# Optimization experiments

Hardware: AMD Instinct MI355X
Metric: run time of the kernel (lower is better)

Reference implementation:

```python
import jax, jax.numpy as jnp
import numpy as np

# ---- static ragged feature layout (from CTGAN metadata) ----
NUM_CLUSTERS = [10, 8, 10, 5, 10, 10, 7, 10, 10, 10]          # per numerical feature
NUM_CATEGORIES = [2, 5, 10, 3, 50, 4, 2, 8, 100, 6, 2, 3, 12, 5, 2, 30, 4, 9, 2, 7]
TAU = 0.2        # GumbelSoftmax temperature (teras default)
BN_EPS = 1e-3    # keras BatchNormalization default epsilon
LATENT_DIM = 128
BATCH = 65536

_seg, _alpha = [], []
_gid = 0
for c in NUM_CLUSTERS:
    _seg.append(_gid); _alpha.append(True); _gid += 1        # alpha scalar (tanh), own segment
    _seg += [_gid] * c; _alpha += [False] * c; _gid += 1     # beta cluster group (gumbel softmax)
for k in NUM_CATEGORIES:
    _seg += [_gid] * k; _alpha += [False] * k; _gid += 1     # categorical group (gumbel softmax)
SEG = jnp.asarray(np.array(_seg, dtype=np.int32))
ALPHA_MASK = jnp.asarray(np.array(_alpha, dtype=bool))
N_SEG = _gid
DATA_DIM = len(_seg)  # 366


def setup_inputs() -> dict:
    key = jax.random.key(0)
    ks = jax.random.split(key, 8)
    z = jax.random.normal(ks[0], (BATCH, LATENT_DIM), dtype=jnp.float32)
    # pre-sampled standard Gumbel noise for the gumbel-softmax groups
    u = jax.random.uniform(ks[1], (BATCH, DATA_DIM), dtype=jnp.float32, minval=1e-6, maxval=1.0 - 1e-6)
    g = -jnp.log(-jnp.log(u))
    def w(k, fi, fo):
        return jax.random.normal(k, (fi, fo), dtype=jnp.float32) * (1.0 / np.sqrt(fi))
    return {
        "z": z, "g": g,
        "W1": w(ks[2], LATENT_DIM, 256), "b1": jnp.zeros((256,), jnp.float32),
        "gamma1": jnp.ones((256,), jnp.float32), "beta1": jnp.zeros((256,), jnp.float32),
        "W2": w(ks[3], LATENT_DIM + 256, 256), "b2": jnp.zeros((256,), jnp.float32),
        "gamma2": jnp.ones((256,), jnp.float32), "beta2": jnp.zeros((256,), jnp.float32),
        "Wout": w(ks[4], LATENT_DIM + 512, DATA_DIM), "bout": jnp.zeros((DATA_DIM,), jnp.float32),
    }


def _bn_relu(h, gamma, beta):
    # training-mode batch norm (batch statistics), as used while training CTGAN
    mu = jnp.mean(h, axis=0)
    var = jnp.var(h, axis=0)
    return jax.nn.relu((h - mu) * jax.lax.rsqrt(var + BN_EPS) * gamma + beta)


def reference(z, g, W1, b1, gamma1, beta1, W2, b2, gamma2, beta2, Wout, bout):
    # CTGAN residual generator layers: out = concat([relu(bn(dense(x))), x])
    h1 = jnp.concatenate([_bn_relu(z @ W1 + b1, gamma1, beta1), z], axis=1)    # [B, 384]
    h2 = jnp.concatenate([_bn_relu(h1 @ W2 + b2, gamma2, beta2), h1], axis=1)  # [B, 640]
    logits = h2 @ Wout + bout                                                  # [B, 366]

    # ragged per-group gumbel-softmax: segment-wise stable softmax over columns
    zt = ((logits + g) / TAU).T                                   # [D, B]
    m = jax.ops.segment_max(zt, SEG, num_segments=N_SEG)          # [S, B]
    e = jnp.exp(zt - m[SEG])
    s = jax.ops.segment_sum(e, SEG, num_segments=N_SEG)
    soft = (e / s[SEG]).T                                         # [B, D]
    # alpha columns: tanh of raw logits; all other columns: group softmax
    return jnp.where(ALPHA_MASK[None, :], jnp.tanh(logits), soft)
```

## Files before the change

kernel.cpp:

```cpp
#include <hip/hip_runtime.h>

typedef _Float16 half_t;
typedef _Float16 half4 __attribute__((ext_vector_type(4)));
typedef _Float16 half8 __attribute__((ext_vector_type(8)));
typedef float f32x4 __attribute__((ext_vector_type(4)));

#define AS1 __attribute__((address_space(1)))
#define AS3 __attribute__((address_space(3)))

static constexpr int NBATCH = 65536;

__device__ __forceinline__ bool is_alpha(int c) {
  const unsigned long long AM0 =
      (1ull << 0) | (1ull << 11) | (1ull << 20) | (1ull << 31) | (1ull << 37) |
      (1ull << 48) | (1ull << 59);
  const unsigned long long AM1 = (1ull << 3) | (1ull << 14) | (1ull << 25);
  if (c >= 90) return false;
  return (((c < 64) ? (AM0 >> c) : (AM1 >> (c - 64))) & 1ull) != 0ull;
}

__global__ __launch_bounds__(256) void k_cvtz(const float* __restrict__ z,
                                              half_t* __restrict__ dst) {
  size_t i = (size_t)blockIdx.x * 256 + threadIdx.x;
  int row = (int)(i >> 4), c8 = (int)(i & 15) << 3;
  const float* s = z + (size_t)row * 128 + c8;
  float4 v0 = *(const float4*)s;
  float4 v1 = *(const float4*)(s + 4);
  half8 h;
  h[0]=(half_t)v0.x; h[1]=(half_t)v0.y; h[2]=(half_t)v0.z; h[3]=(half_t)v0.w;
  h[4]=(half_t)v1.x; h[5]=(half_t)v1.y; h[6]=(half_t)v1.z; h[7]=(half_t)v1.w;
  *(half8*)(dst + (size_t)row * 640 + c8) = h;
}

__global__ __launch_bounds__(256) void k_transpose(const float* __restrict__ W,
                                                   half_t* __restrict__ Wt,
                                                   int K, int N, int total) {
  int i = blockIdx.x * 256 + threadIdx.x;
  if (i >= total) return;
  int n = i / K;
  int k = i - n * K;
  float v = (n < N) ? W[k * N + n] : 0.f;
  Wt[i] = (half_t)v;
}

template<bool STATS, bool F16OUT>
__global__ __launch_bounds__(256) void k_gemm(
    const half_t* __restrict__ A, int lda, int K,
    const half_t* __restrict__ Bt,
    const float* __restrict__ bias,
    half_t* __restrict__ o16, float* __restrict__ o32, int ldo, int ncreal,
    float* __restrict__ ps, float* __restrict__ pq) {
  __shared__ __align__(16) char smem[32768];
  const int tid  = threadIdx.x;
  const int lane = tid & 63;
  const int w    = tid >> 6;
  const int wr   = w >> 1, wc = w & 1;
  const int ml   = lane & 15, g = lane >> 4;
  const int brow = blockIdx.x * 128;
  const int bcol = blockIdx.y * 128;
  const int sr  = lane >> 3;
  const int scg = (lane & 7) ^ sr;

  f32x4 acc[4][4];
#pragma unroll
  for (int i = 0; i < 4; i++)
#pragma unroll
    for (int j = 0; j < 4; j++) acc[i][j] = (f32x4){0.f, 0.f, 0.f, 0.f};

  const half_t* Abase = A  + (size_t)brow * lda;
  const half_t* Bbase = Bt + (size_t)bcol * K;
  const int nt = K >> 6;

  half_t* As = (half_t*)smem;
  half_t* Bs = (half_t*)(smem + 16384);

  for (int t = 0; t < nt; t++) {
    const int k0 = t * 64;
    if (t) __syncthreads();
#pragma unroll
    for (int it = 0; it < 4; it++) {
      int q = it * 4 + w;
      int r = q * 8 + sr;
      __builtin_amdgcn_global_load_lds(
          (AS1 const void*)(Abase + (size_t)r * lda + k0 + scg * 8),
          (AS3 void*)(As + q * 512), 16, 0, 0);
      __builtin_amdgcn_global_load_lds(
          (AS1 const void*)(Bbase + (size_t)r * K + k0 + scg * 8),
          (AS3 void*)(Bs + q * 512), 16, 0, 0);
    }
    __syncthreads();
#pragma unroll
    for (int t2 = 0; t2 < 2; t2++) {
      const int c4 = t2 * 4 + g;
      half8 af[4], bf[4];
#pragma unroll
      for (int fm = 0; fm < 4; fm++) {
        int row = wr * 64 + fm * 16 + ml;
        af[fm] = *(const half8*)((const char*)As + row * 128 + ((c4 ^ (row & 7)) << 4));
      }
#pragma unroll
      for (int fn = 0; fn < 4; fn++) {
        int row = wc * 64 + fn * 16 + ml;
        bf[fn] = *(const half8*)((const char*)Bs + row * 128 + ((c4 ^ (row & 7)) << 4));
      }
#pragma unroll
      for (int fm = 0; fm < 4; fm++)
#pragma unroll
        for (int fn = 0; fn < 4; fn++)
          acc[fm][fn] = __builtin_amdgcn_mfma_f32_16x16x32_f16(af[fm], bf[fn], acc[fm][fn], 0, 0, 0);
    }
  }
  __syncthreads();

#pragma unroll
  for (int fn = 0; fn < 4; fn++) {
    int col  = wc * 64 + fn * 16 + ml;
    int gcol = bcol + col;
    float bz = (gcol < ncreal) ? bias[gcol] : 0.f;
    float s = 0.f, q = 0.f;
#pragma unroll
    for (int fm = 0; fm < 4; fm++)
#pragma unroll
      for (int rr = 0; rr < 4; rr++) {
        float v = acc[fm][fn][rr] + bz;
        acc[fm][fn][rr] = v;
        if (STATS) { s += v; q += v * v; }
      }
    if (STATS) {
      s += __shfl_xor(s, 16, 64); s += __shfl_xor(s, 32, 64);
      q += __shfl_xor(q, 16, 64); q += __shfl_xor(q, 32, 64);
      if (g == 0) {
        ps[(size_t)gcol * 1024 + blockIdx.x * 2 + wr] = s;
        pq[(size_t)gcol * 1024 + blockIdx.x * 2 + wr] = q;
      }
    }
  }

  if (F16OUT) {
    half_t* so = (half_t*)smem;
#pragma unroll
    for (int fn = 0; fn < 4; fn++)
#pragma unroll
      for (int fm = 0; fm < 4; fm++)
#pragma unroll
        for (int rr = 0; rr < 4; rr++)
          so[(wr * 64 + fm * 16 + g * 4 + rr) * 128 + wc * 64 + fn * 16 + ml] =
              (half_t)acc[fm][fn][rr];
    __syncthreads();
#pragma unroll
    for (int it = 0; it < 8; it++) {
      int r = it * 16 + (tid >> 4);
      int c = (tid & 15) * 8;
      *(half8*)(o16 + (size_t)(brow + r) * ldo + bcol + c) = *(const half8*)&so[r * 128 + c];
    }
  } else {
    float* so = (float*)smem;
    for (int h = 0; h < 2; h++) {
      if (wr == h) {
#pragma unroll
        for (int fn = 0; fn < 4; fn++)
#pragma unroll
          for (int fm = 0; fm < 4; fm++)
#pragma unroll
            for (int rr = 0; rr < 4; rr++)
              so[(fm * 16 + g * 4 + rr) * 128 + wc * 64 + fn * 16 + ml] = acc[fm][fn][rr];
      }
      __syncthreads();
      int r0 = h * 64;
      for (int i = tid; i < 64 * 64; i += 256) {
        int r  = i >> 6;
        int c2 = (i & 63) * 2;
        int gc = bcol + c2;
        if (gc < ncreal) {
          float2 v = *(const float2*)&so[r * 128 + c2];
          if (gc < 90) {
            if (is_alpha(gc))     v.x = tanhf(v.x);
            if (is_alpha(gc + 1)) v.y = tanhf(v.y);
          }
          *(float2*)(o32 + (size_t)(brow + r0 + r) * ldo + gc) = v;
        }
      }
      __syncthreads();
    }
  }
}

__global__ __launch_bounds__(256) void k_bnfinal(
    const float* __restrict__ ps, const float* __restrict__ pq,
    const float* __restrict__ gamma, const float* __restrict__ beta,
    float* __restrict__ sc, float* __restrict__ sh) {
  int c = blockIdx.x, t = threadIdx.x;
  float s = 0.f, q = 0.f;
#pragma unroll
  for (int i = 0; i < 4; i++) {
    s += ps[(size_t)c * 1024 + t + i * 256];
    q += pq[(size_t)c * 1024 + t + i * 256];
  }
#pragma unroll
  for (int o = 1; o < 64; o <<= 1) { s += __shfl_xor(s, o, 64); q += __shfl_xor(q, o, 64); }
  __shared__ float ss[4], qq[4];
  if ((t & 63) == 0) { ss[t >> 6] = s; qq[t >> 6] = q; }
  __syncthreads();
  if (t == 0) {
    s = ss[0] + ss[1] + ss[2] + ss[3];
    q = qq[0] + qq[1] + qq[2] + qq[3];
    float mu   = s * (1.f / NBATCH);
    float var  = fmaxf(q * (1.f / NBATCH) - mu * mu, 0.f);
    float rstd = rsqrtf(var + 1e-3f);
    float a = gamma[c] * rstd;
    sc[c] = a;
    sh[c] = beta[c] - mu * a;
  }
}

__global__ __launch_bounds__(256) void k_bnrelu(half_t* __restrict__ p,
                                                const float* __restrict__ sc,
                                                const float* __restrict__ sh) {
  size_t i = (size_t)blockIdx.x * 256 + threadIdx.x;
  int row = (int)(i >> 5), c8 = (int)(i & 31) << 3;
  half_t* a = p + (size_t)row * 640 + c8;
  half8 v = *(const half8*)a;
  half8 o;
#pragma unroll
  for (int j = 0; j < 8; j++)
    o[j] = (half_t)fmaxf(fmaf((float)v[j], sc[c8 + j], sh[c8 + j]), 0.f);
  *(half8*)a = o;
}

template<int L>
__device__ __forceinline__ void seg_norm(float* __restrict__ zr, int S, int Lr) {
  float v[L];
#pragma unroll
  for (int j = 0; j < L; j++) v[j] = (j < Lr) ? zr[S + j] : -1e30f;
  float m = -1e30f;
#pragma unroll
  for (int j = 0; j < L; j++) m = fmaxf(m, v[j]);
  float s = 0.f;
#pragma unroll
  for (int j = 0; j < L; j++) { float e = __expf(v[j] - m); v[j] = e; s += e; }
  const float inv = 1.0f / s;
#pragma unroll
  for (int j = 0; j < L; j++)
    if (j < Lr) zr[S + j] = v[j] * inv;
}

template<int H>
__device__ __forceinline__ void seg_quad(float* __restrict__ zr, int base, int n) {
  float v[H];
#pragma unroll
  for (int j = 0; j < H; j++) v[j] = (j < n) ? zr[base + j] : -1e30f;
  float m = -1e30f;
#pragma unroll
  for (int j = 0; j < H; j++) m = fmaxf(m, v[j]);
  m = fmaxf(m, __shfl_xor(m, 1, 64));
  m = fmaxf(m, __shfl_xor(m, 2, 64));
  float s = 0.f;
#pragma unroll
  for (int j = 0; j < H; j++) { float e = __expf(v[j] - m); v[j] = e; s += e; }
  s += __shfl_xor(s, 1, 64);
  s += __shfl_xor(s, 2, 64);
  const float inv = 1.0f / s;
#pragma unroll
  for (int j = 0; j < H; j++)
    if (j < n) zr[base + j] = v[j] * inv;
}

__global__ __launch_bounds__(256, 6) void k_softmax(const float* __restrict__ g,
                                                    float* __restrict__ out) {
  __shared__ float zb[16][373];
  const int tid = threadIdx.x;
  const size_t gbase = (size_t)blockIdx.x * 16 * 366;
  for (int i2 = tid; i2 < 16 * 183; i2 += 256) {
    int e0 = i2 * 2;
    int r = e0 / 366;
    int c = e0 - r * 366;
    float2 lg = *(const float2*)(out + gbase + e0);
    float2 gg = *(const float2*)(g + gbase + e0);
    zb[r][c]     = is_alpha(c)     ? lg.x : (lg.x + gg.x) * 5.0f;
    zb[r][c + 1] = is_alpha(c + 1) ? lg.y : (lg.y + gg.y) * 5.0f;
  }
  __syncthreads();
  {
    const int lane = tid & 63;
    const int w    = tid >> 6;
    const int quad = lane & 3;
    float* zr = &zb[lane >> 2][0];
    switch (w) {
      case 0:
        seg_quad<25>(zr, 184 + quad * 25, 25);
        break;
      case 1:
        seg_quad<13>(zr, 120 + quad * 13 - (quad >> 1) * (quad & 1), 13 - (quad >> 1));
        seg_quad<8>(zr, 314 + quad * 8 - (quad >> 1) * (quad & 1), 8 - (quad >> 1));
        break;
      case 2: {
        int s0 = (quad == 0) ? 295 : (quad == 1) ? 107 : (quad == 2) ? 38 : 68;
        int l0 = (quad == 0) ? 12 : 10;
        int s1 = (quad == 0) ? 1 : (quad == 1) ? 21 : (quad == 2) ? 49 : 79;
        int s2 = (quad == 0) ? 0 : (quad == 1) ? 100 : (quad == 2) ? 174 : 290;
        int l2 = (quad == 0) ? 0 : 2;
        seg_norm<12>(zr, s0, l0);
        seg_norm<10>(zr, s1, 10);
        seg_norm<2>(zr, s2, l2);
        break;
      }
      default: {
        int s0 = (quad == 0) ? 90 : (quad == 1) ? 12 : (quad == 2) ? 60 : 102;
        int l0 = (quad == 0) ? 10 : (quad == 1) ? 8 : (quad == 2) ? 7 : 5;
        int s1 = (quad == 0) ? 348 : (quad == 1) ? 176 : (quad == 2) ? 359 : 307;
        int l1 = (quad == 0) ? 9 : (quad == 1) ? 8 : (quad == 2) ? 7 : 5;
        int s2 = (quad == 0) ? 312 : (quad == 1) ? 284 : (quad == 2) ? 32 : 170;
        int l2 = (quad == 0) ? 2 : (quad == 1) ? 6 : (quad == 2) ? 5 : 4;
        int s3 = (quad == 0) ? 117 : (quad == 1) ? 357 : (quad == 2) ? 292 : 344;
        int l3 = (quad == 0) ? 3 : (quad == 1) ? 2 : (quad == 2) ? 3 : 4;
        seg_norm<10>(zr, s0, l0);
        seg_norm<9>(zr, s1, l1);
        seg_norm<6>(zr, s2, l2);
        seg_norm<4>(zr, s3, l3);
        break;
      }
    }
  }
  __syncthreads();
  for (int i2 = tid; i2 < 16 * 183; i2 += 256) {
    int e0 = i2 * 2;
    int r = e0 / 366;
    int c = e0 - r * 366;
    float2 v;
    v.x = zb[r][c];
    v.y = zb[r][c + 1];
    *(float2*)(out + gbase + e0) = v;
  }
}

extern "C" void kernel_launch(void* const* d_in, const int* in_sizes, int n_in,
                              void* d_out, int out_size, void* d_ws, size_t ws_size,
                              hipStream_t stream) {
  const float* z      = (const float*)d_in[0];
  const float* g      = (const float*)d_in[1];
  const float* W1     = (const float*)d_in[2];
  const float* b1     = (const float*)d_in[3];
  const float* gamma1 = (const float*)d_in[4];
  const float* beta1  = (const float*)d_in[5];
  const float* W2     = (const float*)d_in[6];
  const float* b2     = (const float*)d_in[7];
  const float* gamma2 = (const float*)d_in[8];
  const float* beta2  = (const float*)d_in[9];
  const float* Wout   = (const float*)d_in[10];
  const float* bout   = (const float*)d_in[11];
  float* out = (float*)d_out;
  char* ws = (char*)d_ws;

  size_t off = 0;
  half_t* act = (half_t*)(ws + off); off += (size_t)NBATCH * 640 * 2;
  half_t* W1t = (half_t*)(ws + off); off += (size_t)256 * 128 * 2;
  half_t* W2t = (half_t*)(ws + off); off += (size_t)256 * 384 * 2;
  half_t* Wot = (half_t*)(ws + off); off += (size_t)384 * 640 * 2;
  float*  ps  = (float*)(ws + off);  off += (size_t)256 * 1024 * 4;
  float*  pq  = (float*)(ws + off);  off += (size_t)256 * 1024 * 4;
  float*  sc1 = (float*)(ws + off);  off += 256 * 4;
  float*  sh1 = (float*)(ws + off);  off += 256 * 4;
  float*  sc2 = (float*)(ws + off);  off += 256 * 4;
  float*  sh2 = (float*)(ws + off);  off += 256 * 4;
  (void)ws_size; (void)in_sizes; (void)n_in; (void)out_size;

  k_cvtz<<<4096, 256, 0, stream>>>(z, act + 512);
  k_transpose<<<(256 * 128 + 255) / 256, 256, 0, stream>>>(W1, W1t, 128, 256, 256 * 128);
  k_transpose<<<(256 * 384 + 255) / 256, 256, 0, stream>>>(W2, W2t, 384, 256, 256 * 384);
  k_transpose<<<(384 * 640 + 255) / 256, 256, 0, stream>>>(Wout, Wot, 640, 366, 384 * 640);

  k_gemm<true, true><<<dim3(512, 2), 256, 0, stream>>>(
      act + 512, 640, 128, W1t, b1, act + 256, nullptr, 640, 256, ps, pq);
  k_bnfinal<<<256, 256, 0, stream>>>(ps, pq, gamma1, beta1, sc1, sh1);
  k_bnrelu<<<8192, 256, 0, stream>>>(act + 256, sc1, sh1);

  k_gemm<true, true><<<dim3(512, 2), 256, 0, stream>>>(
      act + 256, 640, 384, W2t, b2, act + 0, nullptr, 640, 256, ps, pq);
  k_bnfinal<<<256, 256, 0, stream>>>(ps, pq, gamma2, beta2, sc2, sh2);
  k_bnrelu<<<8192, 256, 0, stream>>>(act + 0, sc2, sh2);

  k_gemm<false, false><<<dim3(512, 3), 256, 0, stream>>>(
      act, 640, 640, Wot, bout, nullptr, out, 366, 366, nullptr, nullptr);

  k_softmax<<<NBATCH / 16, 256, 0, stream>>>(g, out);
}
```

Before: 201.4 us.

## Fuse BN+ReLU into next GEMM's A-fragment load and emit fp16 logits

Removes the two standalone BN+ReLU passes over the activation buffer. The per-column affine and ReLU are applied to A fragments inside the following GEMM, using fp16 scale, shift and clamp tables; identity tables cover the raw-z and h1 pass-through columns. The output GEMM now writes fp16 logits (with tanh on alpha columns) into a padded scratch buffer that the softmax kernel reads, instead of writing fp32 into the output. This cuts global traffic and kernel launches, at the cost of extra VALU work per tile, fp16 rounding of the BN parameters and logits, and the same BN being recomputed for every tile.

```diff
diff --git a/kernel.cpp b/kernel.cpp
--- a/kernel.cpp
+++ b/kernel.cpp
@@ -17,6 +17,13 @@
   const unsigned long long AM1 = (1ull << 3) | (1ull << 14) | (1ull << 25);
   if (c >= 90) return false;
   return (((c < 64) ? (AM0 >> c) : (AM1 >> (c - 64))) & 1ull) != 0ull;
+}
+
+__device__ __forceinline__ half8 bn8(half8 x, half8 sc, half8 sh, half8 lo) {
+  half8 r = x * sc + sh;
+#pragma unroll
+  for (int j = 0; j < 8; j++) r[j] = (r[j] < lo[j]) ? lo[j] : r[j];
+  return r;
 }
 
 __global__ __launch_bounds__(256) void k_cvtz(const float* __restrict__ z,
@@ -43,12 +50,19 @@
   Wt[i] = (half_t)v;
 }
 
-template<bool STATS, bool F16OUT>
+__global__ void k_identtab(half_t* sc, half_t* sh, half_t* lo, int n) {
+  int t = blockIdx.x * 128 + threadIdx.x;
+  if (t < n) { sc[t] = (half_t)1.f; sh[t] = (half_t)0.f; lo[t] = (half_t)(-65504.f); }
+}
+
+template<bool STATS, bool TRANS, bool ALPHA>
 __global__ __launch_bounds__(256) void k_gemm(
     const half_t* __restrict__ A, int lda, int K,
     const half_t* __restrict__ Bt,
     const float* __restrict__ bias,
-    half_t* __restrict__ o16, float* __restrict__ o32, int ldo, int ncreal,
+    const half_t* __restrict__ tsc, const half_t* __restrict__ tsh,
+    const half_t* __restrict__ tlo,
+    half_t* __restrict__ o16, int ldo, int ncreal,
     float* __restrict__ ps, float* __restrict__ pq) {
   __shared__ __align__(16) char smem[32768];
   const int tid  = threadIdx.x;
@@ -76,6 +90,12 @@
 
   for (int t = 0; t < nt; t++) {
     const int k0 = t * 64;
+    half8 sc0, sh0, lo0, sc1, sh1, lo1;
+    if (TRANS) {
+      const int ka = k0 + g * 8, kb = k0 + 32 + g * 8;
+      sc0 = *(const half8*)&tsc[ka]; sh0 = *(const half8*)&tsh[ka]; lo0 = *(const half8*)&tlo[ka];
+      sc1 = *(const half8*)&tsc[kb]; sh1 = *(const half8*)&tsh[kb]; lo1 = *(const half8*)&tlo[kb];
+    }
     if (t) __syncthreads();
 #pragma unroll
     for (int it = 0; it < 4; it++) {
@@ -98,6 +118,13 @@
         int row = wr * 64 + fm * 16 + ml;
         af[fm] = *(const half8*)((const char*)As + row * 128 + ((c4 ^ (row & 7)) << 4));
       }
+      if (TRANS) {
+        const half8 sc = t2 ? sc1 : sc0;
+        const half8 sh = t2 ? sh1 : sh0;
+        const half8 lo = t2 ? lo1 : lo0;
+#pragma unroll
+        for (int fm = 0; fm < 4; fm++) af[fm] = bn8(af[fm], sc, sh, lo);
+      }
 #pragma unroll
       for (int fn = 0; fn < 4; fn++) {
         int row = wc * 64 + fn * 16 + ml;
@@ -118,13 +145,15 @@
     int gcol = bcol + col;
     float bz = (gcol < ncreal) ? bias[gcol] : 0.f;
     float s = 0.f, q = 0.f;
+    const bool al = ALPHA && (gcol < 90) && is_alpha(gcol);
 #pragma unroll
     for (int fm = 0; fm < 4; fm++)
 #pragma unroll
       for (int rr = 0; rr < 4; rr++) {
         float v = acc[fm][fn][rr] + bz;
+        if (STATS) { s += v; q += v * v; }
+        if (al) v = tanhf(v);
         acc[fm][fn][rr] = v;
-        if (STATS) { s += v; q += v * v; }
       }
     if (STATS) {
       s += __shfl_xor(s, 16, 64); s += __shfl_xor(s, 32, 64);
@@ -136,59 +165,29 @@
     }
   }
 
-  if (F16OUT) {
-    half_t* so = (half_t*)smem;
-#pragma unroll
-    for (int fn = 0; fn < 4; fn++)
-#pragma unroll
-      for (int fm = 0; fm < 4; fm++)
-#pragma unroll
-        for (int rr = 0; rr < 4; rr++)
-          so[(wr * 64 + fm * 16 + g * 4 + rr) * 128 + wc * 64 + fn * 16 + ml] =
-              (half_t)acc[fm][fn][rr];
-    __syncthreads();
-#pragma unroll
-    for (int it = 0; it < 8; it++) {
-      int r = it * 16 + (tid >> 4);
-      int c = (tid & 15) * 8;
-      *(half8*)(o16 + (size_t)(brow + r) * ldo + bcol + c) = *(const half8*)&so[r * 128 + c];
-    }
-  } else {
-    float* so = (float*)smem;
-    for (int h = 0; h < 2; h++) {
-      if (wr == h) {
-#pragma unroll
-        for (int fn = 0; fn < 4; fn++)
-#pragma unroll
-          for (int fm = 0; fm < 4; fm++)
-#pragma unroll
-            for (int rr = 0; rr < 4; rr++)
-              so[(fm * 16 + g * 4 + rr) * 128 + wc * 64 + fn * 16 + ml] = acc[fm][fn][rr];
-      }
-      __syncthreads();
-      int r0 = h * 64;
-      for (int i = tid; i < 64 * 64; i += 256) {
-        int r  = i >> 6;
-        int c2 = (i & 63) * 2;
-        int gc = bcol + c2;
-        if (gc < ncreal) {
-          float2 v = *(const float2*)&so[r * 128 + c2];
-          if (gc < 90) {
-            if (is_alpha(gc))     v.x = tanhf(v.x);
-            if (is_alpha(gc + 1)) v.y = tanhf(v.y);
-          }
-          *(float2*)(o32 + (size_t)(brow + r0 + r) * ldo + gc) = v;
-        }
-      }
-      __syncthreads();
-    }
+  half_t* so = (half_t*)smem;
+#pragma unroll
+  for (int fn = 0; fn < 4; fn++)
+#pragma unroll
+    for (int fm = 0; fm < 4; fm++)
+#pragma unroll
+      for (int rr = 0; rr < 4; rr++)
+        so[(wr * 64 + fm * 16 + g * 4 + rr) * 128 + wc * 64 + fn * 16 + ml] =
+            (half_t)acc[fm][fn][rr];
+  __syncthreads();
+#pragma unroll
+  for (int it = 0; it < 8; it++) {
+    int r = it * 16 + (tid >> 4);
+    int c = (tid & 15) * 8;
+    *(half8*)(o16 + (size_t)(brow + r) * ldo + bcol + c) = *(const half8*)&so[r * 128 + c];
   }
 }
 
 __global__ __launch_bounds__(256) void k_bnfinal(
     const float* __restrict__ ps, const float* __restrict__ pq,
     const float* __restrict__ gamma, const float* __restrict__ beta,
-    float* __restrict__ sc, float* __restrict__ sh) {
+    half_t* __restrict__ scA, half_t* __restrict__ shA, half_t* __restrict__ loA,
+    half_t* __restrict__ scB, half_t* __restrict__ shB, half_t* __restrict__ loB) {
   int c = blockIdx.x, t = threadIdx.x;
   float s = 0.f, q = 0.f;
 #pragma unroll
@@ -207,24 +206,11 @@
     float mu   = s * (1.f / NBATCH);
     float var  = fmaxf(q * (1.f / NBATCH) - mu * mu, 0.f);
     float rstd = rsqrtf(var + 1e-3f);
-    float a = gamma[c] * rstd;
-    sc[c] = a;
-    sh[c] = beta[c] - mu * a;
-  }
-}
-
-__global__ __launch_bounds__(256) void k_bnrelu(half_t* __restrict__ p,
-                                                const float* __restrict__ sc,
-                                                const float* __restrict__ sh) {
-  size_t i = (size_t)blockIdx.x * 256 + threadIdx.x;
-  int row = (int)(i >> 5), c8 = (int)(i & 31) << 3;
-  half_t* a = p + (size_t)row * 640 + c8;
-  half8 v = *(const half8*)a;
-  half8 o;
-#pragma unroll
-  for (int j = 0; j < 8; j++)
-    o[j] = (half_t)fmaxf(fmaf((float)v[j], sc[c8 + j], sh[c8 + j]), 0.f);
-  *(half8*)a = o;
+    float a  = gamma[c] * rstd;
+    float sh = beta[c] - mu * a;
+    scA[c] = (half_t)a; shA[c] = (half_t)sh; loA[c] = (half_t)0.f;
+    if (scB) { scB[c] = (half_t)a; shB[c] = (half_t)sh; loB[c] = (half_t)0.f; }
+  }
 }
 
 template<int L>
@@ -265,19 +251,22 @@
     if (j < n) zr[base + j] = v[j] * inv;
 }
 
-__global__ __launch_bounds__(256, 6) void k_softmax(const float* __restrict__ g,
+__global__ __launch_bounds__(256, 6) void k_softmax(const half_t* __restrict__ lg,
+                                                    const float* __restrict__ g,
                                                     float* __restrict__ out) {
   __shared__ float zb[16][373];
-  const int tid = threadIdx.x;
-  const size_t gbase = (size_t)blockIdx.x * 16 * 366;
+  const int tid  = threadIdx.x;
+  const int row0 = blockIdx.x * 16;
+  const size_t gbase = (size_t)row0 * 366;
   for (int i2 = tid; i2 < 16 * 183; i2 += 256) {
     int e0 = i2 * 2;
     int r = e0 / 366;
     int c = e0 - r * 366;
-    float2 lg = *(const float2*)(out + gbase + e0);
+    const half_t* lp = lg + (size_t)(row0 + r) * 384 + c;
+    float lx = (float)lp[0], ly = (float)lp[1];
     float2 gg = *(const float2*)(g + gbase + e0);
-    zb[r][c]     = is_alpha(c)     ? lg.x : (lg.x + gg.x) * 5.0f;
-    zb[r][c + 1] = is_alpha(c + 1) ? lg.y : (lg.y + gg.y) * 5.0f;
+    zb[r][c]     = is_alpha(c)     ? lx : (lx + gg.x) * 5.0f;
+    zb[r][c + 1] = is_alpha(c + 1) ? ly : (ly + gg.y) * 5.0f;
   }
   __syncthreads();
   {
@@ -353,34 +342,42 @@
 
   size_t off = 0;
   half_t* act = (half_t*)(ws + off); off += (size_t)NBATCH * 640 * 2;
+  half_t* lg  = (half_t*)(ws + off); off += (size_t)NBATCH * 384 * 2;
   half_t* W1t = (half_t*)(ws + off); off += (size_t)256 * 128 * 2;
   half_t* W2t = (half_t*)(ws + off); off += (size_t)256 * 384 * 2;
   half_t* Wot = (half_t*)(ws + off); off += (size_t)384 * 640 * 2;
   float*  ps  = (float*)(ws + off);  off += (size_t)256 * 1024 * 4;
   float*  pq  = (float*)(ws + off);  off += (size_t)256 * 1024 * 4;
-  float*  sc1 = (float*)(ws + off);  off += 256 * 4;
-  float*  sh1 = (float*)(ws + off);  off += 256 * 4;
-  float*  sc2 = (float*)(ws + off);  off += 256 * 4;
-  float*  sh2 = (float*)(ws + off);  off += 256 * 4;
+  half_t* t2sc = (half_t*)(ws + off); off += 1024;
+  half_t* t2sh = (half_t*)(ws + off); off += 1024;
+  half_t* t2lo = (half_t*)(ws + off); off += 1024;
+  half_t* t3sc = (half_t*)(ws + off); off += 2048;
+  half_t* t3sh = (half_t*)(ws + off); off += 2048;
+  half_t* t3lo = (half_t*)(ws + off); off += 2048;
   (void)ws_size; (void)in_sizes; (void)n_in; (void)out_size;
 
   k_cvtz<<<4096, 256, 0, stream>>>(z, act + 512);
   k_transpose<<<(256 * 128 + 255) / 256, 256, 0, stream>>>(W1, W1t, 128, 256, 256 * 128);
   k_transpose<<<(256 * 384 + 255) / 256, 256, 0, stream>>>(W2, W2t, 384, 256, 256 * 384);
   k_transpose<<<(384 * 640 + 255) / 256, 256, 0, stream>>>(Wout, Wot, 640, 366, 384 * 640);
-
-  k_gemm<true, true><<<dim3(512, 2), 256, 0, stream>>>(
-      act + 512, 640, 128, W1t, b1, act + 256, nullptr, 640, 256, ps, pq);
-  k_bnfinal<<<256, 256, 0, stream>>>(ps, pq, gamma1, beta1, sc1, sh1);
-  k_bnrelu<<<8192, 256, 0, stream>>>(act + 256, sc1, sh1);
-
-  k_gemm<true, true><<<dim3(512, 2), 256, 0, stream>>>(
-      act + 256, 640, 384, W2t, b2, act + 0, nullptr, 640, 256, ps, pq);
-  k_bnfinal<<<256, 256, 0, stream>>>(ps, pq, gamma2, beta2, sc2, sh2);
-  k_bnrelu<<<8192, 256, 0, stream>>>(act + 0, sc2, sh2);
-
-  k_gemm<false, false><<<dim3(512, 3), 256, 0, stream>>>(
-      act, 640, 640, Wot, bout, nullptr, out, 366, 366, nullptr, nullptr);
-
-  k_softmax<<<NBATCH / 16, 256, 0, stream>>>(g, out);
-}
+  k_identtab<<<1, 128, 0, stream>>>(t2sc + 256, t2sh + 256, t2lo + 256, 128);
+  k_identtab<<<1, 128, 0, stream>>>(t3sc + 512, t3sh + 512, t3lo + 512, 128);
+
+  k_gemm<true, false, false><<<dim3(512, 2), 256, 0, stream>>>(
+      act + 512, 640, 128, W1t, b1, nullptr, nullptr, nullptr,
+      act + 256, 640, 256, ps, pq);
+  k_bnfinal<<<256, 256, 0, stream>>>(ps, pq, gamma1, beta1,
+                                     t2sc, t2sh, t2lo, t3sc + 256, t3sh + 256, t3lo + 256);
+
+  k_gemm<true, true, false><<<dim3(512, 2), 256, 0, stream>>>(
+      act + 256, 640, 384, W2t, b2, t2sc, t2sh, t2lo,
+      act + 0, 640, 256, ps, pq);
+  k_bnfinal<<<256, 256, 0, stream>>>(ps, pq, gamma2, beta2,
+                                     t3sc, t3sh, t3lo, nullptr, nullptr, nullptr);
+
+  k_gemm<false, true, true><<<dim3(512, 3), 256, 0, stream>>>(
+      act, 640, 640, Wot, bout, t3sc, t3sh, t3lo,
+      lg, 384, 366, nullptr, nullptr);
+
+  k_softmax<<<NBATCH / 16, 256, 0, stream>>>(lg, g, out);
+}
```

New measurement: 199.5 us. About the same (-1.0%).
